# Kernel optimization log

Hardware: AMD Instinct MI355X
Metric: run time of the kernel (lower is better)

Reference implementation:

```python
import jax, jax.numpy as jnp
import numpy as np

N = 100000
D = 128
H = 128
E = 1600000


def setup_inputs() -> dict:
    key = jax.random.key(0)
    ks = jax.random.split(key, 9)
    x = jax.random.normal(ks[0], (N, D), dtype=jnp.float32)
    edge_index = jax.random.randint(ks[1], (2, E), 0, N, dtype=jnp.int64)
    s = 1.0 / np.sqrt(D)
    W1 = jax.random.uniform(ks[2], (D, H), jnp.float32, -s, s)
    b1 = jnp.zeros((H,), jnp.float32)
    s2 = 1.0 / np.sqrt(H)
    W2 = jax.random.uniform(ks[3], (H, H), jnp.float32, -s2, s2)
    b2 = jnp.zeros((H,), jnp.float32)
    Wo = jax.random.uniform(ks[4], (H, 1), jnp.float32, -s2, s2)
    bo = jax.random.uniform(ks[5], (1,), jnp.float32, -s2, s2)
    return {"x": x, "edge_index": edge_index, "W1": W1, "b1": b1,
            "W2": W2, "b2": b2, "Wo": Wo, "bo": bo}


def _gcn_layer(x, W, b, src, dst, dinv):
    # PyG GCNConv: h = x @ W; out = D^-1/2 (A+I) D^-1/2 h + b
    h = x @ W                                   # [N, H]
    norm = dinv[src] * dinv[dst]                # [E]
    msg = h[src] * norm[:, None]                # [E, H] gathered messages
    agg = jax.ops.segment_sum(msg, dst, num_segments=N)
    agg = agg + h * (dinv * dinv)[:, None]      # self-loop contribution
    return agg + b


def reference(x, edge_index, W1, b1, W2, b2, Wo, bo):
    src, dst = edge_index[0], edge_index[1]
    # degree with self-loops, counted on destination (col), edge_weight = 1
    deg = jax.ops.segment_sum(jnp.ones((E,), jnp.float32), dst, num_segments=N) + 1.0
    dinv = deg ** -0.5                          # [N]
    h = jax.nn.relu(_gcn_layer(x, W1, b1, src, dst, dinv))
    h = _gcn_layer(h, W2, b2, src, dst, dinv)
    out = h @ Wo + bo                            # [N, 1]
    return out[:, 0]                             # [N]
```

## Files before the change

kernel.cpp:

```cpp
#include <hip/hip_runtime.h>
#include <hip/hip_fp16.h>

#define DIM 128
#define NPB 256
#define BCAP 5120
#define T_SCAT 4096

typedef _Float16 half8 __attribute__((ext_vector_type(8)));
typedef float floatx4 __attribute__((ext_vector_type(4)));
typedef float floatx2 __attribute__((ext_vector_type(2)));

__device__ __forceinline__ void gemm_block(const float* __restrict__ X,
                                           const __half* __restrict__ w1frag,
                                           unsigned char* __restrict__ A,
                                           int N, int gb) {
    const int t = threadIdx.x;
    const int w = t >> 6, l = t & 63;
    const int q = l >> 4;
    const int node = gb * 64 + w * 16 + (l & 15);
    const bool valid = node < N;
    half8 bfrag[4];
#pragma unroll
    for (int ks = 0; ks < 4; ks++) {
        float4 f0 = make_float4(0, 0, 0, 0), f1 = make_float4(0, 0, 0, 0);
        if (valid) {
            const float* px = X + (size_t)node * DIM + ks * 32 + q * 8;
            f0 = *(const float4*)px;
            f1 = *(const float4*)(px + 4);
        }
        bfrag[ks][0] = (_Float16)f0.x; bfrag[ks][1] = (_Float16)f0.y;
        bfrag[ks][2] = (_Float16)f0.z; bfrag[ks][3] = (_Float16)f0.w;
        bfrag[ks][4] = (_Float16)f1.x; bfrag[ks][5] = (_Float16)f1.y;
        bfrag[ks][6] = (_Float16)f1.z; bfrag[ks][7] = (_Float16)f1.w;
    }
    const half8* wf = (const half8*)w1frag;
#pragma unroll
    for (int ct = 0; ct < 8; ct++) {
        floatx4 acc = {0.f, 0.f, 0.f, 0.f};
#pragma unroll
        for (int ks = 0; ks < 4; ks++) {
            half8 afrag = wf[(ct * 4 + ks) * 64 + l];
            acc = __builtin_amdgcn_mfma_f32_16x16x32_f16(afrag, bfrag[ks], acc, 0, 0, 0);
        }
        if (valid) {
            int st = 0;
            st = __builtin_amdgcn_cvt_pk_fp8_f32(acc[0], acc[1], st, false);
            st = __builtin_amdgcn_cvt_pk_fp8_f32(acc[2], acc[3], st, true);
            *(int*)(A + (size_t)node * DIM + ct * 16 + q * 4) = st;
        }
    }
}

__global__ void prep_k(const float* __restrict__ W1, const float* __restrict__ W2,
                       const float* __restrict__ Wo, const float* __restrict__ b2,
                       const float* __restrict__ bo,
                       __half* __restrict__ w1frag, float* __restrict__ w2o,
                       float* __restrict__ cbuf, int* __restrict__ bcur) {
    if (blockIdx.x < 8) {
        int idx = blockIdx.x * 256 + threadIdx.x;
        int ct = idx >> 8, ks = (idx >> 6) & 3, l = idx & 63;
        int m = l & 15, q = l >> 4;
        half8 vals;
#pragma unroll
        for (int j = 0; j < 8; j++)
            vals[j] = (_Float16)W1[(ks * 32 + q * 8 + j) * DIM + ct * 16 + m];
        ((half8*)w1frag)[idx] = vals;
    } else if (blockIdx.x == 8) {
        int t = threadIdx.x;
        if (t < 128) {
            float s = 0.f;
            for (int k = 0; k < 128; k++) s += W2[t * 128 + k] * Wo[k];
            w2o[t] = s;
        }
        if (t == 0) {
            float c = bo[0];
            for (int k = 0; k < 128; k++) c += b2[k] * Wo[k];
            cbuf[0] = c;
        }
    } else {
#pragma unroll
        for (int i = 0; i < 4; i++) bcur[threadIdx.x + i * 256] = 0;
    }
}

__global__ __launch_bounds__(256) void scatter_gemm_k(
        const int* __restrict__ ei, int E, int ntiles,
        int2* __restrict__ be, int* __restrict__ bcur,
        const float* __restrict__ X, const __half* __restrict__ w1frag,
        unsigned char* __restrict__ A, int N) {
    if (blockIdx.x >= (unsigned)ntiles) {
        gemm_block(X, w1frag, A, N, blockIdx.x - ntiles);
        return;
    }
    __shared__ int lcnt[1024];
    __shared__ int lscan[1024];
    __shared__ int lbase[1024];
    __shared__ int wsum[4];
    __shared__ int2 stage[T_SCAT];
    const int t = threadIdx.x;
    const int lane = t & 63, w = t >> 6;
    const int tile0 = blockIdx.x * T_SCAT;
    int tcnt = E - tile0; if (tcnt > T_SCAT) tcnt = T_SCAT;
    for (int i = t; i < 1024; i += 256) lcnt[i] = 0;
    __syncthreads();
    for (int i = t; i < tcnt; i += 256)
        atomicAdd(&lcnt[ei[E + tile0 + i] >> 8], 1);
    __syncthreads();
    const int b4 = t * 4;
    int c0 = lcnt[b4], c1 = lcnt[b4 + 1], c2 = lcnt[b4 + 2], c3 = lcnt[b4 + 3];
    int s4 = c0 + c1 + c2 + c3;
    int v = s4;
#pragma unroll
    for (int off = 1; off < 64; off <<= 1) {
        int u = __shfl_up(v, off, 64);
        if (lane >= off) v += u;
    }
    if (lane == 63) wsum[w] = v;
    __syncthreads();
    int wbase = 0;
#pragma unroll
    for (int i = 0; i < 4; i++) wbase += (i < w) ? wsum[i] : 0;
    int run = wbase + v - s4;
    lscan[b4] = run;
    if (c0) lbase[b4] = b4 * BCAP + atomicAdd(&bcur[b4], c0);
    run += c0; lscan[b4 + 1] = run;
    if (c1) lbase[b4 + 1] = (b4 + 1) * BCAP + atomicAdd(&bcur[b4 + 1], c1);
    run += c1; lscan[b4 + 2] = run;
    if (c2) lbase[b4 + 2] = (b4 + 2) * BCAP + atomicAdd(&bcur[b4 + 2], c2);
    run += c2; lscan[b4 + 3] = run;
    if (c3) lbase[b4 + 3] = (b4 + 3) * BCAP + atomicAdd(&bcur[b4 + 3], c3);
    lcnt[b4] = 0; lcnt[b4 + 1] = 0; lcnt[b4 + 2] = 0; lcnt[b4 + 3] = 0;
    __syncthreads();
    for (int i = t; i < tcnt; i += 256) {
        int s = ei[tile0 + i];
        int d = ei[E + tile0 + i];
        int b = d >> 8;
        int r = atomicAdd(&lcnt[b], 1);
        stage[lscan[b] + r] = make_int2(s, d);
    }
    __syncthreads();
    for (int i = t; i < tcnt; i += 256) {
        int2 ed = stage[i];
        int b = ed.y >> 8;
        be[lbase[b] + (i - lscan[b])] = ed;
    }
}

__global__ __launch_bounds__(256) void sort_gemm_k(
        const int2* __restrict__ be, const int* __restrict__ bcur,
        int* __restrict__ csr, int* __restrict__ rp, int* __restrict__ re,
        float* __restrict__ dinv, int N, int nb,
        const float* __restrict__ X, const __half* __restrict__ w1frag,
        unsigned char* __restrict__ A, int gemmBase) {
    if (blockIdx.x >= (unsigned)nb) {
        gemm_block(X, w1frag, A, N, gemmBase + blockIdx.x - nb);
        return;
    }
    __shared__ int lcnt[256];
    __shared__ int lscan[256];
    __shared__ int lc2[256];
    __shared__ int wsum[4];
    __shared__ int stage[BCAP];
    const int t = threadIdx.x;
    const int lane = t & 63, w = t >> 6;
    const int b = blockIdx.x;
    const int s = b * BCAP;
    int cnt = bcur[b]; if (cnt > BCAP) cnt = BCAP;
    lcnt[t] = 0; lc2[t] = 0;
    __syncthreads();
    for (int i = t; i < cnt; i += 256)
        atomicAdd(&lcnt[be[s + i].y & 255], 1);
    __syncthreads();
    int v = lcnt[t];
    int iv = v;
#pragma unroll
    for (int off = 1; off < 64; off <<= 1) {
        int u = __shfl_up(iv, off, 64);
        if (lane >= off) iv += u;
    }
    if (lane == 63) wsum[w] = iv;
    __syncthreads();
    int wbase = 0;
#pragma unroll
    for (int i = 0; i < 4; i++) wbase += (i < w) ? wsum[i] : 0;
    int excl = wbase + iv - v;
    lscan[t] = excl;
    int node = b * NPB + t;
    if (node < N) {
        rp[node] = s + excl;
        re[node] = s + excl + v;
        dinv[node] = rsqrtf((float)v + 1.0f);
    }
    __syncthreads();
    for (int i = t; i < cnt; i += 256) {
        int2 ed = be[s + i];
        int d = ed.y & 255;
        int r = atomicAdd(&lc2[d], 1);
        stage[lscan[d] + r] = ed.x;
    }
    __syncthreads();
    for (int i = t; i < cnt; i += 256) csr[s + i] = stage[i];
}

__device__ __forceinline__ void dec8(int2 r, float* f) {
    floatx2 a = __builtin_amdgcn_cvt_pk_f32_fp8(r.x, false);
    floatx2 b = __builtin_amdgcn_cvt_pk_f32_fp8(r.x, true);
    floatx2 c = __builtin_amdgcn_cvt_pk_f32_fp8(r.y, false);
    floatx2 d = __builtin_amdgcn_cvt_pk_f32_fp8(r.y, true);
    f[0] = a[0]; f[1] = a[1]; f[2] = b[0]; f[3] = b[1];
    f[4] = c[0]; f[5] = c[1]; f[6] = d[0]; f[7] = d[1];
}

__global__ __launch_bounds__(256) void agg1_k(const unsigned char* __restrict__ A,
                                              const int* __restrict__ rp,
                                              const int* __restrict__ re,
                                              const int* __restrict__ csr_src,
                                              const float* __restrict__ dinv,
                                              const float* __restrict__ b1,
                                              const float* __restrict__ w2o,
                                              float* __restrict__ z, int N) {
    const int li = threadIdx.x & 31;
    const int node = blockIdx.x * 8 + (threadIdx.x >> 5);
    if (node >= N) return;
    const int eoff = (li & 15) * 8;
    const float dn = dinv[node];
    const int s0 = rp[node], s1 = re[node];
    float acc[8];
    {
        int2 raw = *(const int2*)(A + (size_t)node * DIM + eoff);
        float hv[8]; dec8(raw, hv);
        float w0 = (li < 16) ? dn * dn : 0.f;
#pragma unroll
        for (int e = 0; e < 8; e++) acc[e] = hv[e] * w0;
    }
    for (int base = s0; base < s1; base += 32) {
        int sidx = 0; float dsl = 0.f;
        if (base + li < s1) { sidx = csr_src[base + li]; dsl = dinv[sidx]; }
        int nloc = s1 - base; if (nloc > 32) nloc = 32;
        int npair = (nloc + 1) >> 1;
#pragma unroll 2
        for (int j = 0; j < npair; j++) {
            int sel = 2 * j + (li >> 4);
            int ssrc = __shfl(sidx, sel, 32);
            float wgt = __shfl(dsl, sel, 32) * dn;
            int2 hraw = *(const int2*)(A + (size_t)ssrc * DIM + eoff);
            float h[8]; dec8(hraw, h);
#pragma unroll
            for (int e = 0; e < 8; e++) acc[e] = fmaf(h[e], wgt, acc[e]);
        }
    }
#pragma unroll
    for (int e = 0; e < 8; e++) acc[e] += __shfl_xor(acc[e], 16, 32);
    float sum = 0.f;
    if (li < 16) {
        float4 b0 = *(const float4*)(b1 + eoff);
        float4 b3 = *(const float4*)(b1 + eoff + 4);
        float4 w0 = *(const float4*)(w2o + eoff);
        float4 w3 = *(const float4*)(w2o + eoff + 4);
        sum  = fmaxf(acc[0] + b0.x, 0.f) * w0.x;
        sum += fmaxf(acc[1] + b0.y, 0.f) * w0.y;
        sum += fmaxf(acc[2] + b0.z, 0.f) * w0.z;
        sum += fmaxf(acc[3] + b0.w, 0.f) * w0.w;
        sum += fmaxf(acc[4] + b3.x, 0.f) * w3.x;
        sum += fmaxf(acc[5] + b3.y, 0.f) * w3.y;
        sum += fmaxf(acc[6] + b3.z, 0.f) * w3.z;
        sum += fmaxf(acc[7] + b3.w, 0.f) * w3.w;
    }
#pragma unroll
    for (int off = 16; off > 0; off >>= 1) sum += __shfl_down(sum, off, 32);
    if (li == 0) z[node] = sum;
}

__global__ void final_k(const float* __restrict__ z, const float* __restrict__ dinv,
                        const int* __restrict__ rp, const int* __restrict__ re,
                        const int* __restrict__ csr_src,
                        const float* __restrict__ cbuf, float* __restrict__ out, int N) {
    int n = blockIdx.x * 256 + threadIdx.x;
    if (n >= N) return;
    float dn = dinv[n];
    int s0 = rp[n], s1 = re[n];
    float s = 0.f;
    for (int i = s0; i < s1; i++) {
        int sx = csr_src[i];
        s = fmaf(dinv[sx], z[sx], s);
    }
    out[n] = fmaf(dn, s, fmaf(dn * dn, z[n], cbuf[0]));
}

extern "C" void kernel_launch(void* const* d_in, const int* in_sizes, int n_in,
                              void* d_out, int out_size, void* d_ws, size_t ws_size,
                              hipStream_t stream) {
    const float* x  = (const float*)d_in[0];
    const int*   ei = (const int*)d_in[1];
    const float* W1 = (const float*)d_in[2];
    const float* b1 = (const float*)d_in[3];
    const float* W2 = (const float*)d_in[4];
    const float* b2 = (const float*)d_in[5];
    const float* Wo = (const float*)d_in[6];
    const float* bo = (const float*)d_in[7];
    float* out = (float*)d_out;

    const int N = in_sizes[0] / DIM;
    const int E = in_sizes[1] / 2;
    const int NB = (N + NPB - 1) >> 8;
    const int ntiles = (E + T_SCAT - 1) / T_SCAT;
    const int ngemm = (N + 63) / 64;
    const int g1 = ngemm / 2;
    const int g2 = ngemm - g1;

    char* p = (char*)d_ws;
    auto alloc = [&](size_t bytes) {
        void* r = (void*)p;
        p += (bytes + 255) & ~size_t(255);
        return r;
    };
    unsigned char* A = (unsigned char*)alloc((size_t)N * DIM);
    int2*  be     = (int2*)alloc((size_t)NB * BCAP * 8);
    int*   csr    = (int*)alloc((size_t)NB * BCAP * 4);
    float* z      = (float*)alloc((size_t)N * 4);
    float* dinv   = (float*)alloc((size_t)N * 4);
    float* w2o    = (float*)alloc(128 * 4);
    float* cbuf   = (float*)alloc(16);
    __half* w1frag= (__half*)alloc(2048 * 8 * 2);
    int* rp       = (int*)alloc((size_t)N * 4);
    int* re       = (int*)alloc((size_t)N * 4);
    int* bcur     = (int*)alloc(1024 * 4);

    prep_k<<<10, 256, 0, stream>>>(W1, W2, Wo, b2, bo, w1frag, w2o, cbuf, bcur);
    scatter_gemm_k<<<ntiles + g1, 256, 0, stream>>>(ei, E, ntiles, be, bcur,
                                                    x, w1frag, A, N);
    sort_gemm_k<<<NB + g2, 256, 0, stream>>>(be, bcur, csr, rp, re, dinv, N, NB,
                                             x, w1frag, A, g1);
    agg1_k<<<(N + 7) / 8, 256, 0, stream>>>(A, rp, re, csr, dinv, b1, w2o, z, N);
    final_k<<<(N + 255) / 256, 256, 0, stream>>>(z, dinv, rp, re, csr, cbuf, out, N);
}
```

Before: 232.2 us.

## Batch edge loads, prefetch gathers, fold dinv scaling, move GEMM into scatter kernel

Edge-index and bucket loads in the scatter and sort kernels are batched so several global loads are in flight before the shared-memory atomics. The agg1 gather loop is software-pipelined so the next row is fetched while the current one is accumulated. The per-edge dinv[dst] multiply is factored out and applied once per node, and agg1 stores dinv-prescaled z so final_k no longer gathers dinv per edge and is unrolled by four. All GEMM blocks now launch with the scatter kernel instead of half running with sort, which reorders the overlap between the stages.

```diff
diff --git a/kernel.cpp b/kernel.cpp
--- a/kernel.cpp
+++ b/kernel.cpp
@@ -103,8 +103,18 @@
     int tcnt = E - tile0; if (tcnt > T_SCAT) tcnt = T_SCAT;
     for (int i = t; i < 1024; i += 256) lcnt[i] = 0;
     __syncthreads();
-    for (int i = t; i < tcnt; i += 256)
-        atomicAdd(&lcnt[ei[E + tile0 + i] >> 8], 1);
+    for (int base = 0; base < tcnt; base += 1024) {
+        int i0 = base + t;
+        int d0 = -1, d1 = -1, d2 = -1, d3 = -1;
+        if (i0       < tcnt) d0 = ei[E + tile0 + i0];
+        if (i0 + 256 < tcnt) d1 = ei[E + tile0 + i0 + 256];
+        if (i0 + 512 < tcnt) d2 = ei[E + tile0 + i0 + 512];
+        if (i0 + 768 < tcnt) d3 = ei[E + tile0 + i0 + 768];
+        if (d0 >= 0) atomicAdd(&lcnt[d0 >> 8], 1);
+        if (d1 >= 0) atomicAdd(&lcnt[d1 >> 8], 1);
+        if (d2 >= 0) atomicAdd(&lcnt[d2 >> 8], 1);
+        if (d3 >= 0) atomicAdd(&lcnt[d3 >> 8], 1);
+    }
     __syncthreads();
     const int b4 = t * 4;
     int c0 = lcnt[b4], c1 = lcnt[b4 + 1], c2 = lcnt[b4 + 2], c3 = lcnt[b4 + 3];
@@ -131,12 +141,22 @@
     if (c3) lbase[b4 + 3] = (b4 + 3) * BCAP + atomicAdd(&bcur[b4 + 3], c3);
     lcnt[b4] = 0; lcnt[b4 + 1] = 0; lcnt[b4 + 2] = 0; lcnt[b4 + 3] = 0;
     __syncthreads();
-    for (int i = t; i < tcnt; i += 256) {
-        int s = ei[tile0 + i];
-        int d = ei[E + tile0 + i];
-        int b = d >> 8;
-        int r = atomicAdd(&lcnt[b], 1);
-        stage[lscan[b] + r] = make_int2(s, d);
+    for (int base = 0; base < tcnt; base += 512) {
+        int i0 = base + t, i1 = i0 + 256;
+        bool v0 = i0 < tcnt, v1 = i1 < tcnt;
+        int s0 = 0, d0 = 0, s1 = 0, d1 = 0;
+        if (v0) { s0 = ei[tile0 + i0]; d0 = ei[E + tile0 + i0]; }
+        if (v1) { s1 = ei[tile0 + i1]; d1 = ei[E + tile0 + i1]; }
+        if (v0) {
+            int b = d0 >> 8;
+            int r = atomicAdd(&lcnt[b], 1);
+            stage[lscan[b] + r] = make_int2(s0, d0);
+        }
+        if (v1) {
+            int b = d1 >> 8;
+            int r = atomicAdd(&lcnt[b], 1);
+            stage[lscan[b] + r] = make_int2(s1, d1);
+        }
     }
     __syncthreads();
     for (int i = t; i < tcnt; i += 256) {
@@ -146,16 +166,10 @@
     }
 }
 
-__global__ __launch_bounds__(256) void sort_gemm_k(
+__global__ __launch_bounds__(256) void sort_k(
         const int2* __restrict__ be, const int* __restrict__ bcur,
         int* __restrict__ csr, int* __restrict__ rp, int* __restrict__ re,
-        float* __restrict__ dinv, int N, int nb,
-        const float* __restrict__ X, const __half* __restrict__ w1frag,
-        unsigned char* __restrict__ A, int gemmBase) {
-    if (blockIdx.x >= (unsigned)nb) {
-        gemm_block(X, w1frag, A, N, gemmBase + blockIdx.x - nb);
-        return;
-    }
+        float* __restrict__ dinv, int N) {
     __shared__ int lcnt[256];
     __shared__ int lscan[256];
     __shared__ int lc2[256];
@@ -168,8 +182,18 @@
     int cnt = bcur[b]; if (cnt > BCAP) cnt = BCAP;
     lcnt[t] = 0; lc2[t] = 0;
     __syncthreads();
-    for (int i = t; i < cnt; i += 256)
-        atomicAdd(&lcnt[be[s + i].y & 255], 1);
+    for (int base = 0; base < cnt; base += 1024) {
+        int i0 = base + t;
+        int y0 = -1, y1 = -1, y2 = -1, y3 = -1;
+        if (i0       < cnt) y0 = be[s + i0].y;
+        if (i0 + 256 < cnt) y1 = be[s + i0 + 256].y;
+        if (i0 + 512 < cnt) y2 = be[s + i0 + 512].y;
+        if (i0 + 768 < cnt) y3 = be[s + i0 + 768].y;
+        if (y0 >= 0) atomicAdd(&lcnt[y0 & 255], 1);
+        if (y1 >= 0) atomicAdd(&lcnt[y1 & 255], 1);
+        if (y2 >= 0) atomicAdd(&lcnt[y2 & 255], 1);
+        if (y3 >= 0) atomicAdd(&lcnt[y3 & 255], 1);
+    }
     __syncthreads();
     int v = lcnt[t];
     int iv = v;
@@ -192,11 +216,22 @@
         dinv[node] = rsqrtf((float)v + 1.0f);
     }
     __syncthreads();
-    for (int i = t; i < cnt; i += 256) {
-        int2 ed = be[s + i];
-        int d = ed.y & 255;
-        int r = atomicAdd(&lc2[d], 1);
-        stage[lscan[d] + r] = ed.x;
+    for (int base = 0; base < cnt; base += 512) {
+        int i0 = base + t, i1 = i0 + 256;
+        bool v0 = i0 < cnt, v1 = i1 < cnt;
+        int2 e0, e1;
+        if (v0) e0 = be[s + i0];
+        if (v1) e1 = be[s + i1];
+        if (v0) {
+            int d = e0.y & 255;
+            int r = atomicAdd(&lc2[d], 1);
+            stage[lscan[d] + r] = e0.x;
+        }
+        if (v1) {
+            int d = e1.y & 255;
+            int r = atomicAdd(&lc2[d], 1);
+            stage[lscan[d] + r] = e1.x;
+        }
     }
     __syncthreads();
     for (int i = t; i < cnt; i += 256) csr[s + i] = stage[i];
@@ -218,7 +253,7 @@
                                               const float* __restrict__ dinv,
                                               const float* __restrict__ b1,
                                               const float* __restrict__ w2o,
-                                              float* __restrict__ z, int N) {
+                                              float* __restrict__ zp, int N) {
     const int li = threadIdx.x & 31;
     const int node = blockIdx.x * 8 + (threadIdx.x >> 5);
     if (node >= N) return;
@@ -229,7 +264,7 @@
     {
         int2 raw = *(const int2*)(A + (size_t)node * DIM + eoff);
         float hv[8]; dec8(raw, hv);
-        float w0 = (li < 16) ? dn * dn : 0.f;
+        float w0 = (li < 16) ? dn : 0.f;
 #pragma unroll
         for (int e = 0; e < 8; e++) acc[e] = hv[e] * w0;
     }
@@ -238,16 +273,23 @@
         if (base + li < s1) { sidx = csr_src[base + li]; dsl = dinv[sidx]; }
         int nloc = s1 - base; if (nloc > 32) nloc = 32;
         int npair = (nloc + 1) >> 1;
-#pragma unroll 2
-        for (int j = 0; j < npair; j++) {
-            int sel = 2 * j + (li >> 4);
-            int ssrc = __shfl(sidx, sel, 32);
-            float wgt = __shfl(dsl, sel, 32) * dn;
-            int2 hraw = *(const int2*)(A + (size_t)ssrc * DIM + eoff);
+        int sel = (li >> 4);
+        int ssrc = __shfl(sidx, sel, 32);
+        float wgt = __shfl(dsl, sel, 32);
+        int2 hraw = *(const int2*)(A + (size_t)ssrc * DIM + eoff);
+        for (int j = 1; j < npair; j++) {
+            int sel1 = 2 * j + (li >> 4);
+            int ssrc1 = __shfl(sidx, sel1, 32);
+            float wgt1 = __shfl(dsl, sel1, 32);
+            int2 hnext = *(const int2*)(A + (size_t)ssrc1 * DIM + eoff);
             float h[8]; dec8(hraw, h);
 #pragma unroll
             for (int e = 0; e < 8; e++) acc[e] = fmaf(h[e], wgt, acc[e]);
-        }
+            hraw = hnext; wgt = wgt1;
+        }
+        float h[8]; dec8(hraw, h);
+#pragma unroll
+        for (int e = 0; e < 8; e++) acc[e] = fmaf(h[e], wgt, acc[e]);
     }
 #pragma unroll
     for (int e = 0; e < 8; e++) acc[e] += __shfl_xor(acc[e], 16, 32);
@@ -257,21 +299,21 @@
         float4 b3 = *(const float4*)(b1 + eoff + 4);
         float4 w0 = *(const float4*)(w2o + eoff);
         float4 w3 = *(const float4*)(w2o + eoff + 4);
-        sum  = fmaxf(acc[0] + b0.x, 0.f) * w0.x;
-        sum += fmaxf(acc[1] + b0.y, 0.f) * w0.y;
-        sum += fmaxf(acc[2] + b0.z, 0.f) * w0.z;
-        sum += fmaxf(acc[3] + b0.w, 0.f) * w0.w;
-        sum += fmaxf(acc[4] + b3.x, 0.f) * w3.x;
-        sum += fmaxf(acc[5] + b3.y, 0.f) * w3.y;
-        sum += fmaxf(acc[6] + b3.z, 0.f) * w3.z;
-        sum += fmaxf(acc[7] + b3.w, 0.f) * w3.w;
+        sum  = fmaxf(fmaf(dn, acc[0], b0.x), 0.f) * w0.x;
+        sum += fmaxf(fmaf(dn, acc[1], b0.y), 0.f) * w0.y;
+        sum += fmaxf(fmaf(dn, acc[2], b0.z), 0.f) * w0.z;
+        sum += fmaxf(fmaf(dn, acc[3], b0.w), 0.f) * w0.w;
+        sum += fmaxf(fmaf(dn, acc[4], b3.x), 0.f) * w3.x;
+        sum += fmaxf(fmaf(dn, acc[5], b3.y), 0.f) * w3.y;
+        sum += fmaxf(fmaf(dn, acc[6], b3.z), 0.f) * w3.z;
+        sum += fmaxf(fmaf(dn, acc[7], b3.w), 0.f) * w3.w;
     }
 #pragma unroll
     for (int off = 16; off > 0; off >>= 1) sum += __shfl_down(sum, off, 32);
-    if (li == 0) z[node] = sum;
-}
-
-__global__ void final_k(const float* __restrict__ z, const float* __restrict__ dinv,
+    if (li == 0) zp[node] = dn * sum;
+}
+
+__global__ void final_k(const float* __restrict__ zp, const float* __restrict__ dinv,
                         const int* __restrict__ rp, const int* __restrict__ re,
                         const int* __restrict__ csr_src,
                         const float* __restrict__ cbuf, float* __restrict__ out, int N) {
@@ -280,11 +322,14 @@
     float dn = dinv[n];
     int s0 = rp[n], s1 = re[n];
     float s = 0.f;
-    for (int i = s0; i < s1; i++) {
-        int sx = csr_src[i];
-        s = fmaf(dinv[sx], z[sx], s);
-    }
-    out[n] = fmaf(dn, s, fmaf(dn * dn, z[n], cbuf[0]));
+    int i = s0;
+    for (; i + 4 <= s1; i += 4) {
+        int x0 = csr_src[i], x1 = csr_src[i + 1], x2 = csr_src[i + 2], x3 = csr_src[i + 3];
+        float z0 = zp[x0], z1 = zp[x1], z2 = zp[x2], z3 = zp[x3];
+        s += (z0 + z1) + (z2 + z3);
+    }
+    for (; i < s1; i++) s += zp[csr_src[i]];
+    out[n] = fmaf(dn, s + zp[n], cbuf[0]);
 }
 
 extern "C" void kernel_launch(void* const* d_in, const int* in_sizes, int n_in,
@@ -305,8 +350,6 @@
     const int NB = (N + NPB - 1) >> 8;
     const int ntiles = (E + T_SCAT - 1) / T_SCAT;
     const int ngemm = (N + 63) / 64;
-    const int g1 = ngemm / 2;
-    const int g2 = ngemm - g1;
 
     char* p = (char*)d_ws;
     auto alloc = [&](size_t bytes) {
@@ -317,7 +360,7 @@
     unsigned char* A = (unsigned char*)alloc((size_t)N * DIM);
     int2*  be     = (int2*)alloc((size_t)NB * BCAP * 8);
     int*   csr    = (int*)alloc((size_t)NB * BCAP * 4);
-    float* z      = (float*)alloc((size_t)N * 4);
+    float* zp     = (float*)alloc((size_t)N * 4);
     float* dinv   = (float*)alloc((size_t)N * 4);
     float* w2o    = (float*)alloc(128 * 4);
     float* cbuf   = (float*)alloc(16);
@@ -327,10 +370,9 @@
     int* bcur     = (int*)alloc(1024 * 4);
 
     prep_k<<<10, 256, 0, stream>>>(W1, W2, Wo, b2, bo, w1frag, w2o, cbuf, bcur);
-    scatter_gemm_k<<<ntiles + g1, 256, 0, stream>>>(ei, E, ntiles, be, bcur,
-                                                    x, w1frag, A, N);
-    sort_gemm_k<<<NB + g2, 256, 0, stream>>>(be, bcur, csr, rp, re, dinv, N, NB,
-                                             x, w1frag, A, g1);
-    agg1_k<<<(N + 7) / 8, 256, 0, stream>>>(A, rp, re, csr, dinv, b1, w2o, z, N);
-    final_k<<<(N + 255) / 256, 256, 0, stream>>>(z, dinv, rp, re, csr, cbuf, out, N);
-}
+    scatter_gemm_k<<<ntiles + ngemm, 256, 0, stream>>>(ei, E, ntiles, be, bcur,
+                                                       x, w1frag, A, N);
+    sort_k<<<NB, 256, 0, stream>>>(be, bcur, csr, rp, re, dinv, N);
+    agg1_k<<<(N + 7) / 8, 256, 0, stream>>>(A, rp, re, csr, dinv, b1, w2o, zp, N);
+    final_k<<<(N + 255) / 256, 256, 0, stream>>>(zp, dinv, rp, re, csr, cbuf, out, N);
+}
```

After: 220.0 us. -5.3%, faster.
